# Kernel optimization log

Measured on AMD Instinct MI355X. Metric: run time of the kernel, lower is better.

Reference implementation:

```python
import jax, jax.numpy as jnp
import numpy as np


def gcn_conv(x, W, b, src, dst, w, num_nodes):
    """PyG GCNConv: out = D^{-1/2} (A + I) D^{-1/2} (x @ W) + b, edge weights w."""
    xw = x @ W  # [BN, out_dim]
    # degree with self-loop weight 1.0, accumulated at target nodes
    deg = jax.ops.segment_sum(w, dst, num_segments=num_nodes) + 1.0  # [BN]
    dinv = jax.lax.rsqrt(deg)
    norm = dinv[src] * w * dinv[dst]  # [E]
    agg = jax.ops.segment_sum(xw[src] * norm[:, None], dst, num_segments=num_nodes)
    agg = agg + xw * (dinv * dinv)[:, None]  # self-loop contribution
    return agg + b


def setup_inputs() -> dict:
    key = jax.random.key(0)
    ks = jax.random.split(key, 10)
    BN, E, D = 100000, 1600000, 128
    return {
        "x": jax.random.normal(ks[0], (BN, D), dtype=jnp.float32),
        "edge_index": jax.random.randint(ks[1], (2, E), 0, BN, dtype=jnp.int64),
        "B": 8,
        "N": 12500,
        "causal_edge_index": jax.random.randint(ks[2], (2, 16), 0, BN, dtype=jnp.int64),
        "edge_weight": jax.random.uniform(ks[3], (E,), dtype=jnp.float32),
        "causal_edge_weight": jax.random.uniform(ks[4], (16,), dtype=jnp.float32),
        "W1": jax.random.normal(ks[5], (D, D), dtype=jnp.float32) * (1.0 / np.sqrt(D)),
        "b1": jnp.zeros((D,), dtype=jnp.float32),
        "W2": jax.random.normal(ks[6], (D, D), dtype=jnp.float32) * (1.0 / np.sqrt(D)),
        "b2": jnp.zeros((D,), dtype=jnp.float32),
        "Wres": jax.random.normal(ks[7], (D, D), dtype=jnp.float32) * (1.0 / np.sqrt(D)),
        "bres": jnp.zeros((D,), dtype=jnp.float32),
    }


def reference(x, edge_index, B, N, causal_edge_index, edge_weight,
              causal_edge_weight, W1, b1, W2, b2, Wres, bres):
    BN = B * N
    src, dst = edge_index[0], edge_index[1]
    # layer 1: GCNConv -> gelu (dropout is identity in eval)
    h = gcn_conv(x, W1, b1, src, dst, edge_weight, BN)  # [BN, hidden]
    h = jax.nn.gelu(h, approximate=False)
    # residual: 0.3 * Linear(x)
    h = h + 0.3 * (x @ Wres + bres)
    # layer 2: GCNConv -> gelu
    out = gcn_conv(h, W2, b2, src, dst, edge_weight, BN)
    return jax.nn.gelu(out, approximate=False)
```

## Files before the change

### kernel.cpp

```cpp
#include <hip/hip_runtime.h>
#include <math.h>

#define DIM 128
#define SCAN_CHUNK 4096

typedef __attribute__((ext_vector_type(8))) short short8;
typedef __attribute__((ext_vector_type(4))) float f32x4;

__device__ __forceinline__ float gelu_exact(float v) {
    return 0.5f * v * (1.0f + erff(v * 0.70710678118654752f));
}

__device__ __forceinline__ unsigned short f2bf(float f) {
    unsigned int u = __float_as_uint(f);
    return (unsigned short)((u + 0x7FFFu + ((u >> 16) & 1u)) >> 16);
}
__device__ __forceinline__ float bf_lo(unsigned int v) { return __uint_as_float(v << 16); }
__device__ __forceinline__ float bf_hi(unsigned int v) { return __uint_as_float(v & 0xFFFF0000u); }


__global__ void deg_cnt_kernel(const int* __restrict__ dst,
                               const float* __restrict__ w,
                               unsigned long long* __restrict__ packed,
                               int* __restrict__ rank, int E) {
    int e = blockIdx.x * blockDim.x + threadIdx.x;
    if (e >= E) return;
    int d = dst[e];
    unsigned long long inc =
        (1ull << 32) | (unsigned long long)(unsigned int)(w[e] * 67108864.0f);
    unsigned long long old = atomicAdd(&packed[d], inc);
    rank[e] = (int)(old >> 32);
}

__global__ void dinv_kernel(const unsigned long long* __restrict__ packed,
                            float* __restrict__ dinvf, int* __restrict__ cnt, int BN) {
    int n = blockIdx.x * blockDim.x + threadIdx.x;
    if (n >= BN) return;
    unsigned long long v = packed[n];
    cnt[n] = (int)(v >> 32);
    float sum = (float)(unsigned int)(v & 0xFFFFFFFFu) * (1.0f / 67108864.0f);
    dinvf[n] = rsqrtf(sum + 1.0f);
}

__global__ __launch_bounds__(256) void scanA_kernel(const int* __restrict__ cnt,
                                                    int* __restrict__ partials, int BN) {
    int tid = threadIdx.x;
    int base = blockIdx.x * SCAN_CHUNK;
    int sum = 0;
#pragma unroll
    for (int i = 0; i < 16; i++) {
        int ii = base + i * 256 + tid;
        if (ii < BN) sum += cnt[ii];
    }
    __shared__ int lds[4];
#pragma unroll
    for (int off = 32; off; off >>= 1) sum += __shfl_down(sum, off, 64);
    if ((tid & 63) == 0) lds[tid >> 6] = sum;
    __syncthreads();
    if (tid == 0) partials[blockIdx.x] = lds[0] + lds[1] + lds[2] + lds[3];
}

__global__ __launch_bounds__(256) void scanB_kernel(int* __restrict__ partials, int nblk) {
    __shared__ int lds[256];
    int tid = threadIdx.x;
    int v = (tid < nblk) ? partials[tid] : 0;
    lds[tid] = v;
    __syncthreads();
#pragma unroll
    for (int off = 1; off < 256; off <<= 1) {
        int t = (tid >= off) ? lds[tid - off] : 0;
        __syncthreads();
        lds[tid] += t;
        __syncthreads();
    }
    if (tid < nblk) partials[tid] = lds[tid] - v;
}

__global__ __launch_bounds__(256) void scanC_kernel(const int* __restrict__ cnt,
                                                    const int* __restrict__ partials,
                                                    int* __restrict__ ptr, int BN) {
    __shared__ int lds[256];
    int tid = threadIdx.x;
    int base = blockIdx.x * SCAN_CHUNK;
    int idx0 = base + tid * 16;
    int v[16];
    int tsum = 0;
#pragma unroll
    for (int j = 0; j < 16; j++) {
        int ii = idx0 + j;
        v[j] = (ii < BN) ? cnt[ii] : 0;
        tsum += v[j];
    }
    lds[tid] = tsum;
    __syncthreads();
#pragma unroll
    for (int off = 1; off < 256; off <<= 1) {
        int t = (tid >= off) ? lds[tid - off] : 0;
        __syncthreads();
        lds[tid] += t;
        __syncthreads();
    }
    int excl = lds[tid] - tsum + partials[blockIdx.x];
#pragma unroll
    for (int j = 0; j < 16; j++) {
        int ii = idx0 + j;
        if (ii < BN) ptr[ii] = excl;
        excl += v[j];
    }
}

__global__ void fill_kernel(const int* __restrict__ ei, const float* __restrict__ w,
                            const int* __restrict__ rank, const int* __restrict__ ptr,
                            const float* __restrict__ dinvf,
                            int2* __restrict__ csr, int E) {
    int e = blockIdx.x * blockDim.x + threadIdx.x;
    if (e >= E) return;
    int s = ei[e];
    int d = ei[(size_t)E + e];
    int pos = ptr[d] + rank[e];
    float nrm = dinvf[s] * w[e] * dinvf[d];
    csr[pos] = make_int2(s, __float_as_int(nrm));
}


__global__ __launch_bounds__(256) void wt_kernel(const float* __restrict__ W,
                                                 unsigned short* __restrict__ Wt) {
    int idx = blockIdx.x * 256 + threadIdx.x;
    int r = idx >> 7, c = idx & 127;
    Wt[c * 128 + r] = f2bf(W[idx]);
}


template <int MODE>
__global__ __launch_bounds__(256) void mfma_gemm_kernel(const float* __restrict__ X,
                                                        const unsigned short* __restrict__ Wt,
                                                        const float* __restrict__ bias,
                                                        unsigned short* __restrict__ outb,
                                                        float* __restrict__ Bf, int BN) {
    int tid = threadIdx.x;
    int w = tid >> 6, l = tid & 63;
    int l15 = l & 15, kg = l >> 4;
    int row0 = blockIdx.x * 64 + w * 16;

    int rowA = row0 + l15;
    if (rowA > BN - 1) rowA = BN - 1;
    const float* ap = X + (size_t)rowA * 128 + kg * 8;

    f32x4 acc[8];
#pragma unroll
    for (int nt = 0; nt < 8; nt++) acc[nt] = (f32x4){0.f, 0.f, 0.f, 0.f};

#pragma unroll
    for (int ks = 0; ks < 4; ks++) {
        float4 a0 = *(const float4*)(ap + ks * 32);
        float4 a1 = *(const float4*)(ap + ks * 32 + 4);
        short8 aF;
        aF[0] = (short)f2bf(a0.x); aF[1] = (short)f2bf(a0.y);
        aF[2] = (short)f2bf(a0.z); aF[3] = (short)f2bf(a0.w);
        aF[4] = (short)f2bf(a1.x); aF[5] = (short)f2bf(a1.y);
        aF[6] = (short)f2bf(a1.z); aF[7] = (short)f2bf(a1.w);
#pragma unroll
        for (int nt = 0; nt < 8; nt++) {
            int colB = nt * 16 + l15;
            uint4 bu = *(const uint4*)(Wt + (size_t)colB * 128 + ks * 32 + kg * 8);
            short8 bF = __builtin_bit_cast(short8, bu);
            acc[nt] = __builtin_amdgcn_mfma_f32_16x16x32_bf16(aF, bF, acc[nt], 0, 0, 0);
        }
    }

#pragma unroll
    for (int nt = 0; nt < 8; nt++) {
        int col = nt * 16 + l15;
#pragma unroll
        for (int r = 0; r < 4; r++) {
            int row = row0 + kg * 4 + r;
            if (row >= BN) continue;
            size_t idx = (size_t)row * 128 + col;
            if (MODE == 0) {
                outb[idx] = f2bf(acc[nt][r]);
            } else {
                Bf[idx] += 0.3f * (acc[nt][r] + bias[col]);
            }
        }
    }
}


__global__ __launch_bounds__(256) void agg_kernel(const unsigned short* __restrict__ XWb,
                                                  const float* __restrict__ dinvf,
                                                  const int* __restrict__ ptr,
                                                  const int* __restrict__ cnt,
                                                  const int2* __restrict__ csr,
                                                  const float* __restrict__ bias,
                                                  float* __restrict__ out, int BN) {
    int h = threadIdx.x >> 5;
    int lane = threadIdx.x & 31;
    int n = blockIdx.x * 8 + h;
    if (n >= BN) return;
    int beg = ptr[n];
    int endv = beg + cnt[n];

    float4 acc0 = make_float4(0.f, 0.f, 0.f, 0.f);
    float4 acc1 = make_float4(0.f, 0.f, 0.f, 0.f);
    int i = beg;
    for (; i + 1 < endv; i += 2) {
        int2 e0 = csr[i];
        int2 e1 = csr[i + 1];
        uint2 r0 = *(const uint2*)(XWb + (size_t)e0.x * 128 + lane * 4);
        uint2 r1 = *(const uint2*)(XWb + (size_t)e1.x * 128 + lane * 4);
        float n0 = __int_as_float(e0.y), n1 = __int_as_float(e1.y);
        acc0.x += n0 * bf_lo(r0.x); acc0.y += n0 * bf_hi(r0.x);
        acc0.z += n0 * bf_lo(r0.y); acc0.w += n0 * bf_hi(r0.y);
        acc1.x += n1 * bf_lo(r1.x); acc1.y += n1 * bf_hi(r1.x);
        acc1.z += n1 * bf_lo(r1.y); acc1.w += n1 * bf_hi(r1.y);
    }
    if (i < endv) {
        int2 e0 = csr[i];
        uint2 r0 = *(const uint2*)(XWb + (size_t)e0.x * 128 + lane * 4);
        float n0 = __int_as_float(e0.y);
        acc0.x += n0 * bf_lo(r0.x); acc0.y += n0 * bf_hi(r0.x);
        acc0.z += n0 * bf_lo(r0.y); acc0.w += n0 * bf_hi(r0.y);
    }
    float dn = dinvf[n];
    float sl = dn * dn;
    uint2 rs = *(const uint2*)(XWb + (size_t)n * 128 + lane * 4);
    float4 bb = ((const float4*)bias)[lane];
    float4 o;
    o.x = gelu_exact(acc0.x + acc1.x + sl * bf_lo(rs.x) + bb.x);
    o.y = gelu_exact(acc0.y + acc1.y + sl * bf_hi(rs.x) + bb.y);
    o.z = gelu_exact(acc0.z + acc1.z + sl * bf_lo(rs.y) + bb.z);
    o.w = gelu_exact(acc0.w + acc1.w + sl * bf_hi(rs.y) + bb.w);
    ((float4*)(out + (size_t)n * 128))[lane] = o;
}


extern "C" void kernel_launch(void* const* d_in, const int* in_sizes, int n_in,
                              void* d_out, int out_size, void* d_ws, size_t ws_size,
                              hipStream_t stream) {
    const float* x = (const float*)d_in[0];
    const int* ei = (const int*)d_in[1];
    const float* w = (const float*)d_in[5];
    const float* W1 = (const float*)d_in[7];
    const float* b1 = (const float*)d_in[8];
    const float* W2 = (const float*)d_in[9];
    const float* b2 = (const float*)d_in[10];
    const float* Wres = (const float*)d_in[11];
    const float* bres = (const float*)d_in[12];

    const int BN = in_sizes[0] / DIM;
    const int E = in_sizes[1] / 2;
    const int NBLK = (BN + SCAN_CHUNK - 1) / SCAN_CHUNK;

    char* p = (char*)d_ws;
    unsigned short* Ab = (unsigned short*)p;         p += (size_t)BN * DIM * 2;
    unsigned long long* packed = (unsigned long long*)p;  p += (size_t)BN * 8;
    float* dinvf = (float*)p;          p += (size_t)BN * 4;
    int* cnt = (int*)p;                p += (size_t)BN * 4;
    int* ptr = (int*)p;                p += (size_t)BN * 4;
    int* partials = (int*)p;           p += 1024;
    unsigned short* Wt1 = (unsigned short*)p;   p += 128 * 128 * 2;
    unsigned short* Wtr = (unsigned short*)p;   p += 128 * 128 * 2;
    unsigned short* Wt2 = (unsigned short*)p;   p += 128 * 128 * 2;
    int* rank = (int*)p;               p += (size_t)E * 4;
    int2* csr = (int2*)p;              p += (size_t)E * 8;

    float* Bf = (float*)d_out;

    const int* dst32 = ei + E;

    hipMemsetAsync(packed, 0, (size_t)BN * 8, stream);

    int tE = (E + 255) / 256;
    int tN = (BN + 255) / 256;

    deg_cnt_kernel<<<tE, 256, 0, stream>>>(dst32, w, packed, rank, E);
    dinv_kernel<<<tN, 256, 0, stream>>>(packed, dinvf, cnt, BN);
    scanA_kernel<<<NBLK, 256, 0, stream>>>(cnt, partials, BN);
    scanB_kernel<<<1, 256, 0, stream>>>(partials, NBLK);
    scanC_kernel<<<NBLK, 256, 0, stream>>>(cnt, partials, ptr, BN);
    fill_kernel<<<tE, 256, 0, stream>>>(ei, w, rank, ptr, dinvf, csr, E);

    wt_kernel<<<64, 256, 0, stream>>>(W1, Wt1);
    wt_kernel<<<64, 256, 0, stream>>>(Wres, Wtr);
    wt_kernel<<<64, 256, 0, stream>>>(W2, Wt2);

    int gemmBlocks = (BN + 63) / 64;
    int aggBlocks = (BN + 7) / 8;

    mfma_gemm_kernel<0><<<gemmBlocks, 256, 0, stream>>>(x, Wt1, nullptr, Ab, nullptr, BN);
    agg_kernel<<<aggBlocks, 256, 0, stream>>>(Ab, dinvf, ptr, cnt, csr, b1, Bf, BN);
    mfma_gemm_kernel<1><<<gemmBlocks, 256, 0, stream>>>(x, Wtr, bres, nullptr, Bf, BN);

    mfma_gemm_kernel<0><<<gemmBlocks, 256, 0, stream>>>(Bf, Wt2, nullptr, Ab, nullptr, BN);
    agg_kernel<<<aggBlocks, 256, 0, stream>>>(Ab, dinvf, ptr, cnt, csr, b2, (float*)d_out, BN);
}
```

Before: 519.6 us.

## Fuse GEMMs with degree counting into one launch and merge scan/dinv kernels

Builds a single phase0 kernel whose blocks run either the x@W1 GEMM, the residual x@Wres GEMM (written directly into the output buffer), or the degree/rank atomic counting. All three pieces of work now share one launch and can overlap. The dinv computation moves into the first scan pass, and the three weight-transpose kernels are merged into one. The aggregation kernel adds its result onto the precomputed residual and is unrolled to four edges per iteration. Together these cut the number of launches and the serial gaps between them, at the cost of heterogeneous blocks inside one grid and higher register use in the aggregation kernel.

```diff
diff --git a/kernel.cpp b/kernel.cpp
--- a/kernel.cpp
+++ b/kernel.cpp
@@ -19,38 +19,133 @@
 __device__ __forceinline__ float bf_hi(unsigned int v) { return __uint_as_float(v & 0xFFFF0000u); }
 
 
-__global__ void deg_cnt_kernel(const int* __restrict__ dst,
-                               const float* __restrict__ w,
-                               unsigned long long* __restrict__ packed,
-                               int* __restrict__ rank, int E) {
-    int e = blockIdx.x * blockDim.x + threadIdx.x;
-    if (e >= E) return;
-    int d = dst[e];
-    unsigned long long inc =
-        (1ull << 32) | (unsigned long long)(unsigned int)(w[e] * 67108864.0f);
-    unsigned long long old = atomicAdd(&packed[d], inc);
-    rank[e] = (int)(old >> 32);
-}
-
-__global__ void dinv_kernel(const unsigned long long* __restrict__ packed,
-                            float* __restrict__ dinvf, int* __restrict__ cnt, int BN) {
-    int n = blockIdx.x * blockDim.x + threadIdx.x;
-    if (n >= BN) return;
-    unsigned long long v = packed[n];
-    cnt[n] = (int)(v >> 32);
-    float sum = (float)(unsigned int)(v & 0xFFFFFFFFu) * (1.0f / 67108864.0f);
-    dinvf[n] = rsqrtf(sum + 1.0f);
-}
-
-__global__ __launch_bounds__(256) void scanA_kernel(const int* __restrict__ cnt,
-                                                    int* __restrict__ partials, int BN) {
+__global__ __launch_bounds__(256) void wt3_kernel(const float* __restrict__ W1,
+                                                  const float* __restrict__ Wres,
+                                                  const float* __restrict__ W2,
+                                                  unsigned short* __restrict__ Wt1,
+                                                  unsigned short* __restrict__ Wtr,
+                                                  unsigned short* __restrict__ Wt2) {
+    int b = blockIdx.x;
+    const float* W = (b < 64) ? W1 : (b < 128) ? Wres : W2;
+    unsigned short* Wt = (b < 64) ? Wt1 : (b < 128) ? Wtr : Wt2;
+    int idx = (b & 63) * 256 + threadIdx.x;
+    int r = idx >> 7, c = idx & 127;
+    Wt[c * 128 + r] = f2bf(W[idx]);
+}
+
+
+template <int MODE>
+__device__ __forceinline__ void gemm_body(const float* __restrict__ X,
+                                          const unsigned short* __restrict__ Wt,
+                                          const float* __restrict__ bias,
+                                          unsigned short* __restrict__ outb,
+                                          float* __restrict__ Bf, int bid, int BN) {
+    int tid = threadIdx.x;
+    int w = tid >> 6, l = tid & 63;
+    int l15 = l & 15, kg = l >> 4;
+    int row0 = bid * 64 + w * 16;
+
+    int rowA = row0 + l15;
+    if (rowA > BN - 1) rowA = BN - 1;
+    const float* ap = X + (size_t)rowA * 128 + kg * 8;
+
+    f32x4 acc[8];
+#pragma unroll
+    for (int nt = 0; nt < 8; nt++) acc[nt] = (f32x4){0.f, 0.f, 0.f, 0.f};
+
+#pragma unroll
+    for (int ks = 0; ks < 4; ks++) {
+        float4 a0 = *(const float4*)(ap + ks * 32);
+        float4 a1 = *(const float4*)(ap + ks * 32 + 4);
+        short8 aF;
+        aF[0] = (short)f2bf(a0.x); aF[1] = (short)f2bf(a0.y);
+        aF[2] = (short)f2bf(a0.z); aF[3] = (short)f2bf(a0.w);
+        aF[4] = (short)f2bf(a1.x); aF[5] = (short)f2bf(a1.y);
+        aF[6] = (short)f2bf(a1.z); aF[7] = (short)f2bf(a1.w);
+#pragma unroll
+        for (int nt = 0; nt < 8; nt++) {
+            int colB = nt * 16 + l15;
+            uint4 bu = *(const uint4*)(Wt + (size_t)colB * 128 + ks * 32 + kg * 8);
+            short8 bF = __builtin_bit_cast(short8, bu);
+            acc[nt] = __builtin_amdgcn_mfma_f32_16x16x32_bf16(aF, bF, acc[nt], 0, 0, 0);
+        }
+    }
+
+#pragma unroll
+    for (int nt = 0; nt < 8; nt++) {
+        int col = nt * 16 + l15;
+#pragma unroll
+        for (int r = 0; r < 4; r++) {
+            int row = row0 + kg * 4 + r;
+            if (row >= BN) continue;
+            size_t idx = (size_t)row * 128 + col;
+            if (MODE == 0) {
+                outb[idx] = f2bf(acc[nt][r]);
+            } else {
+                Bf[idx] = 0.3f * (acc[nt][r] + bias[col]);
+            }
+        }
+    }
+}
+
+template <int MODE>
+__global__ __launch_bounds__(256) void mfma_gemm_kernel(const float* __restrict__ X,
+                                                        const unsigned short* __restrict__ Wt,
+                                                        const float* __restrict__ bias,
+                                                        unsigned short* __restrict__ outb,
+                                                        float* __restrict__ Bf, int BN) {
+    gemm_body<MODE>(X, Wt, bias, outb, Bf, blockIdx.x, BN);
+}
+
+
+__global__ __launch_bounds__(256) void phase0_kernel(const float* __restrict__ x,
+                                                     const unsigned short* __restrict__ Wt1,
+                                                     const unsigned short* __restrict__ Wtr,
+                                                     const float* __restrict__ bres,
+                                                     unsigned short* __restrict__ Ab,
+                                                     float* __restrict__ Bf,
+                                                     const int* __restrict__ dst,
+                                                     const float* __restrict__ w,
+                                                     unsigned long long* __restrict__ packed,
+                                                     int* __restrict__ rank,
+                                                     int BN, int E, int gB) {
+    int b = blockIdx.x;
+    if (b < gB) { gemm_body<0>(x, Wt1, nullptr, Ab, nullptr, b, BN); return; }
+    b -= gB;
+    if (b < gB) { gemm_body<2>(x, Wtr, bres, nullptr, Bf, b, BN); return; }
+    b -= gB;
+    int e0 = b * 512 + threadIdx.x;
+#pragma unroll
+    for (int it = 0; it < 2; it++) {
+        int e = e0 + it * 256;
+        if (e < E) {
+            int d = dst[e];
+            unsigned long long inc =
+                (1ull << 32) | (unsigned long long)(unsigned int)(w[e] * 67108864.0f);
+            unsigned long long old = atomicAdd(&packed[d], inc);
+            rank[e] = (int)(old >> 32);
+        }
+    }
+}
+
+
+__global__ __launch_bounds__(256) void scanAD_kernel(const unsigned long long* __restrict__ packed,
+                                                     float* __restrict__ dinvf,
+                                                     int* __restrict__ cnt,
+                                                     int* __restrict__ partials, int BN) {
     int tid = threadIdx.x;
     int base = blockIdx.x * SCAN_CHUNK;
     int sum = 0;
 #pragma unroll
     for (int i = 0; i < 16; i++) {
         int ii = base + i * 256 + tid;
-        if (ii < BN) sum += cnt[ii];
+        if (ii < BN) {
+            unsigned long long v = packed[ii];
+            int c = (int)(v >> 32);
+            cnt[ii] = c;
+            dinvf[ii] = rsqrtf((float)(unsigned int)(v & 0xFFFFFFFFu) * (1.0f / 67108864.0f) + 1.0f);
+            sum += c;
+        }
     }
     __shared__ int lds[4];
 #pragma unroll
@@ -123,69 +218,7 @@
 }
 
 
-__global__ __launch_bounds__(256) void wt_kernel(const float* __restrict__ W,
-                                                 unsigned short* __restrict__ Wt) {
-    int idx = blockIdx.x * 256 + threadIdx.x;
-    int r = idx >> 7, c = idx & 127;
-    Wt[c * 128 + r] = f2bf(W[idx]);
-}
-
-
-template <int MODE>
-__global__ __launch_bounds__(256) void mfma_gemm_kernel(const float* __restrict__ X,
-                                                        const unsigned short* __restrict__ Wt,
-                                                        const float* __restrict__ bias,
-                                                        unsigned short* __restrict__ outb,
-                                                        float* __restrict__ Bf, int BN) {
-    int tid = threadIdx.x;
-    int w = tid >> 6, l = tid & 63;
-    int l15 = l & 15, kg = l >> 4;
-    int row0 = blockIdx.x * 64 + w * 16;
-
-    int rowA = row0 + l15;
-    if (rowA > BN - 1) rowA = BN - 1;
-    const float* ap = X + (size_t)rowA * 128 + kg * 8;
-
-    f32x4 acc[8];
-#pragma unroll
-    for (int nt = 0; nt < 8; nt++) acc[nt] = (f32x4){0.f, 0.f, 0.f, 0.f};
-
-#pragma unroll
-    for (int ks = 0; ks < 4; ks++) {
-        float4 a0 = *(const float4*)(ap + ks * 32);
-        float4 a1 = *(const float4*)(ap + ks * 32 + 4);
-        short8 aF;
-        aF[0] = (short)f2bf(a0.x); aF[1] = (short)f2bf(a0.y);
-        aF[2] = (short)f2bf(a0.z); aF[3] = (short)f2bf(a0.w);
-        aF[4] = (short)f2bf(a1.x); aF[5] = (short)f2bf(a1.y);
-        aF[6] = (short)f2bf(a1.z); aF[7] = (short)f2bf(a1.w);
-#pragma unroll
-        for (int nt = 0; nt < 8; nt++) {
-            int colB = nt * 16 + l15;
-            uint4 bu = *(const uint4*)(Wt + (size_t)colB * 128 + ks * 32 + kg * 8);
-            short8 bF = __builtin_bit_cast(short8, bu);
-            acc[nt] = __builtin_amdgcn_mfma_f32_16x16x32_bf16(aF, bF, acc[nt], 0, 0, 0);
-        }
-    }
-
-#pragma unroll
-    for (int nt = 0; nt < 8; nt++) {
-        int col = nt * 16 + l15;
-#pragma unroll
-        for (int r = 0; r < 4; r++) {
-            int row = row0 + kg * 4 + r;
-            if (row >= BN) continue;
-            size_t idx = (size_t)row * 128 + col;
-            if (MODE == 0) {
-                outb[idx] = f2bf(acc[nt][r]);
-            } else {
-                Bf[idx] += 0.3f * (acc[nt][r] + bias[col]);
-            }
-        }
-    }
-}
-
-
+template <int ACCMODE>
 __global__ __launch_bounds__(256) void agg_kernel(const unsigned short* __restrict__ XWb,
                                                   const float* __restrict__ dinvf,
                                                   const int* __restrict__ ptr,
@@ -200,37 +233,50 @@
     int beg = ptr[n];
     int endv = beg + cnt[n];
 
-    float4 acc0 = make_float4(0.f, 0.f, 0.f, 0.f);
-    float4 acc1 = make_float4(0.f, 0.f, 0.f, 0.f);
+    float4 a0 = make_float4(0.f, 0.f, 0.f, 0.f);
+    float4 a1 = make_float4(0.f, 0.f, 0.f, 0.f);
+    float4 a2 = make_float4(0.f, 0.f, 0.f, 0.f);
+    float4 a3 = make_float4(0.f, 0.f, 0.f, 0.f);
     int i = beg;
-    for (; i + 1 < endv; i += 2) {
-        int2 e0 = csr[i];
-        int2 e1 = csr[i + 1];
+    for (; i + 3 < endv; i += 4) {
+        int2 e0 = csr[i], e1 = csr[i + 1], e2 = csr[i + 2], e3 = csr[i + 3];
         uint2 r0 = *(const uint2*)(XWb + (size_t)e0.x * 128 + lane * 4);
         uint2 r1 = *(const uint2*)(XWb + (size_t)e1.x * 128 + lane * 4);
+        uint2 r2 = *(const uint2*)(XWb + (size_t)e2.x * 128 + lane * 4);
+        uint2 r3 = *(const uint2*)(XWb + (size_t)e3.x * 128 + lane * 4);
         float n0 = __int_as_float(e0.y), n1 = __int_as_float(e1.y);
-        acc0.x += n0 * bf_lo(r0.x); acc0.y += n0 * bf_hi(r0.x);
-        acc0.z += n0 * bf_lo(r0.y); acc0.w += n0 * bf_hi(r0.y);
-        acc1.x += n1 * bf_lo(r1.x); acc1.y += n1 * bf_hi(r1.x);
-        acc1.z += n1 * bf_lo(r1.y); acc1.w += n1 * bf_hi(r1.y);
-    }
-    if (i < endv) {
+        float n2 = __int_as_float(e2.y), n3 = __int_as_float(e3.y);
+        a0.x += n0 * bf_lo(r0.x); a0.y += n0 * bf_hi(r0.x);
+        a0.z += n0 * bf_lo(r0.y); a0.w += n0 * bf_hi(r0.y);
+        a1.x += n1 * bf_lo(r1.x); a1.y += n1 * bf_hi(r1.x);
+        a1.z += n1 * bf_lo(r1.y); a1.w += n1 * bf_hi(r1.y);
+        a2.x += n2 * bf_lo(r2.x); a2.y += n2 * bf_hi(r2.x);
+        a2.z += n2 * bf_lo(r2.y); a2.w += n2 * bf_hi(r2.y);
+        a3.x += n3 * bf_lo(r3.x); a3.y += n3 * bf_hi(r3.x);
+        a3.z += n3 * bf_lo(r3.y); a3.w += n3 * bf_hi(r3.y);
+    }
+    for (; i < endv; i++) {
         int2 e0 = csr[i];
         uint2 r0 = *(const uint2*)(XWb + (size_t)e0.x * 128 + lane * 4);
         float n0 = __int_as_float(e0.y);
-        acc0.x += n0 * bf_lo(r0.x); acc0.y += n0 * bf_hi(r0.x);
-        acc0.z += n0 * bf_lo(r0.y); acc0.w += n0 * bf_hi(r0.y);
+        a0.x += n0 * bf_lo(r0.x); a0.y += n0 * bf_hi(r0.x);
+        a0.z += n0 * bf_lo(r0.y); a0.w += n0 * bf_hi(r0.y);
     }
     float dn = dinvf[n];
     float sl = dn * dn;
     uint2 rs = *(const uint2*)(XWb + (size_t)n * 128 + lane * 4);
     float4 bb = ((const float4*)bias)[lane];
     float4 o;
-    o.x = gelu_exact(acc0.x + acc1.x + sl * bf_lo(rs.x) + bb.x);
-    o.y = gelu_exact(acc0.y + acc1.y + sl * bf_hi(rs.x) + bb.y);
-    o.z = gelu_exact(acc0.z + acc1.z + sl * bf_lo(rs.y) + bb.z);
-    o.w = gelu_exact(acc0.w + acc1.w + sl * bf_hi(rs.y) + bb.w);
-    ((float4*)(out + (size_t)n * 128))[lane] = o;
+    o.x = gelu_exact(a0.x + a1.x + a2.x + a3.x + sl * bf_lo(rs.x) + bb.x);
+    o.y = gelu_exact(a0.y + a1.y + a2.y + a3.y + sl * bf_hi(rs.x) + bb.y);
+    o.z = gelu_exact(a0.z + a1.z + a2.z + a3.z + sl * bf_lo(rs.y) + bb.z);
+    o.w = gelu_exact(a0.w + a1.w + a2.w + a3.w + sl * bf_hi(rs.y) + bb.w);
+    float4* op = (float4*)(out + (size_t)n * 128) + lane;
+    if (ACCMODE == 1) {
+        float4 prev = *op;
+        o.x += prev.x; o.y += prev.y; o.z += prev.z; o.w += prev.w;
+    }
+    *op = o;
 }
 
 
@@ -271,26 +317,22 @@
     hipMemsetAsync(packed, 0, (size_t)BN * 8, stream);
 
     int tE = (E + 255) / 256;
-    int tN = (BN + 255) / 256;
-
-    deg_cnt_kernel<<<tE, 256, 0, stream>>>(dst32, w, packed, rank, E);
-    dinv_kernel<<<tN, 256, 0, stream>>>(packed, dinvf, cnt, BN);
-    scanA_kernel<<<NBLK, 256, 0, stream>>>(cnt, partials, BN);
+    int gB = (BN + 63) / 64;
+    int degBlocks = (E + 511) / 512;
+    int aggBlocks = (BN + 7) / 8;
+
+    wt3_kernel<<<192, 256, 0, stream>>>(W1, Wres, W2, Wt1, Wtr, Wt2);
+
+    phase0_kernel<<<2 * gB + degBlocks, 256, 0, stream>>>(x, Wt1, Wtr, bres, Ab, Bf,
+                                                          dst32, w, packed, rank, BN, E, gB);
+
+    scanAD_kernel<<<NBLK, 256, 0, stream>>>(packed, dinvf, cnt, partials, BN);
     scanB_kernel<<<1, 256, 0, stream>>>(partials, NBLK);
     scanC_kernel<<<NBLK, 256, 0, stream>>>(cnt, partials, ptr, BN);
     fill_kernel<<<tE, 256, 0, stream>>>(ei, w, rank, ptr, dinvf, csr, E);
 
-    wt_kernel<<<64, 256, 0, stream>>>(W1, Wt1);
-    wt_kernel<<<64, 256, 0, stream>>>(Wres, Wtr);
-    wt_kernel<<<64, 256, 0, stream>>>(W2, Wt2);
-
-    int gemmBlocks = (BN + 63) / 64;
-    int aggBlocks = (BN + 7) / 8;
-
-    mfma_gemm_kernel<0><<<gemmBlocks, 256, 0, stream>>>(x, Wt1, nullptr, Ab, nullptr, BN);
-    agg_kernel<<<aggBlocks, 256, 0, stream>>>(Ab, dinvf, ptr, cnt, csr, b1, Bf, BN);
-    mfma_gemm_kernel<1><<<gemmBlocks, 256, 0, stream>>>(x, Wtr, bres, nullptr, Bf, BN);
-
-    mfma_gemm_kernel<0><<<gemmBlocks, 256, 0, stream>>>(Bf, Wt2, nullptr, Ab, nullptr, BN);
-    agg_kernel<<<aggBlocks, 256, 0, stream>>>(Ab, dinvf, ptr, cnt, csr, b2, (float*)d_out, BN);
-}
+    agg_kernel<1><<<aggBlocks, 256, 0, stream>>>(Ab, dinvf, ptr, cnt, csr, b1, Bf, BN);
+
+    mfma_gemm_kernel<0><<<gB, 256, 0, stream>>>(Bf, Wt2, nullptr, Ab, nullptr, BN);
+    agg_kernel<0><<<aggBlocks, 256, 0, stream>>>(Ab, dinvf, ptr, cnt, csr, b2, (float*)d_out, BN);
+}
```

After: 487.5 us. 1.07x faster.
